# Optimization experiments

Hardware: AMD Instinct MI355X
Metric: run time of the kernel (lower is better)

## Reference

```python
import jax, jax.numpy as jnp
import numpy as np

N, D, C = 8192, 10000, 1000


def setup_inputs() -> dict:
    key = jax.random.key(0)
    k1, k2 = jax.random.split(key)
    # binary {0,1} hypervectors, stored as float32 for efficient GEMM-form Hamming distance
    samples = jax.random.randint(k1, (N, D), 0, 2).astype(jnp.float32)
    classes_hv = jax.random.randint(k2, (C, D), 0, 2).astype(jnp.float32)
    return {"samples": samples, "classes_hv": classes_hv}


def reference(samples, classes_hv):
    # Original: response[i] = sum_d xor(samples[:, d], classes_hv[i, d])  (Hamming distance)
    # For binary a,b: xor(a,b) = a + b - 2*a*b, so the full [N, C] distance matrix is
    # dist = row_sum(samples)[:, None] + row_sum(hv)[None, :] - 2 * samples @ hv.T
    # This replaces the per-class XOR+reduce loop with one GEMM (same math).
    s_sum = jnp.sum(samples, axis=-1)          # [N]
    c_sum = jnp.sum(classes_hv, axis=-1)       # [C]
    cross = jnp.einsum('nd,cd->nc', samples, classes_hv)  # [N, C]
    return s_sum[:, None] + c_sum[None, :] - 2.0 * cross  # [N, C] Hamming distances
```

## Files before the change

### kernel.cpp

```cpp
#include <hip/hip_runtime.h>
#include <stdint.h>

#define N_ROWS 8192
#define C_CLS  1000
#define D_DIM  10000
#define W64P   160
#define W32P   (W64P * 2)
#define DP     (W32P * 32)
#define BKW    16
#define NCHUNK 20

typedef int v4i  __attribute__((ext_vector_type(4)));
typedef int v16i __attribute__((ext_vector_type(16)));

__global__ __launch_bounds__(256) void pack_kernel(
    const float* __restrict__ samples, const float* __restrict__ classes,
    unsigned long long* __restrict__ pA, unsigned long long* __restrict__ pB)
{
    int gwave = (blockIdx.x * 256 + threadIdx.x) >> 6;
    int lane  = threadIdx.x & 63;
    if (gwave >= N_ROWS + C_CLS) return;

    const float* src;
    unsigned long long* dst;
    if (gwave < N_ROWS) {
        src = samples + (size_t)gwave * D_DIM;
        dst = pA + (size_t)gwave * W64P;
    } else {
        int r = gwave - N_ROWS;
        src = classes + (size_t)r * D_DIM;
        dst = pB + (size_t)r * W64P;
    }

    #pragma unroll 4
    for (int w = 0; w < 40; ++w) {
        int idx = w * 256 + lane * 4;
        float4 v = make_float4(0.f, 0.f, 0.f, 0.f);
        if (idx < D_DIM) v = *(const float4*)(src + idx);
        unsigned long long m0 = __ballot(v.x > 0.5f);
        unsigned long long m1 = __ballot(v.y > 0.5f);
        unsigned long long m2 = __ballot(v.z > 0.5f);
        unsigned long long m3 = __ballot(v.w > 0.5f);
        if (lane == 0) {
            uint4 p0, p1;
            p0.x = (uint32_t)m0; p0.y = (uint32_t)(m0 >> 32);
            p0.z = (uint32_t)m1; p0.w = (uint32_t)(m1 >> 32);
            p1.x = (uint32_t)m2; p1.y = (uint32_t)(m2 >> 32);
            p1.z = (uint32_t)m3; p1.w = (uint32_t)(m3 >> 32);
            *(uint4*)(dst + (size_t)w * 4)     = p0;
            *(uint4*)(dst + (size_t)w * 4 + 2) = p1;
        }
    }
}

__global__ __launch_bounds__(256) void hd_kernel(
    const uint32_t* __restrict__ pA, const uint32_t* __restrict__ pB,
    float* __restrict__ out)
{
    __shared__ uint32_t AsT[2][BKW][128];
    __shared__ uint32_t BsT[2][BKW][128];

    const int tid  = threadIdx.x;
    const int row0 = blockIdx.x * 128;
    const int col0 = blockIdx.y * 128;

    const int w    = tid >> 6;
    const int lane = tid & 63;
    const int wy   = w >> 1;
    const int wx   = w & 1;
    const int ln   = lane & 31;
    const int h4   = (lane >> 5) * 4;

    const int srow = tid >> 1;
    const int sq2  = (tid & 1) * 2;
    const uint32_t* gAs = pA + (size_t)(row0 + srow) * W32P + sq2 * 4;
    int gc = col0 + srow; if (gc >= C_CLS) gc = C_CLS - 1;
    const uint32_t* gBs = pB + (size_t)gc * W32P + sq2 * 4;

    uint4 av[2], bv[2];

#define LOADR(ch) do {                                             \
    av[0] = *(const uint4*)(gAs + (ch) * BKW);                     \
    av[1] = *(const uint4*)(gAs + (ch) * BKW + 4);                 \
    bv[0] = *(const uint4*)(gBs + (ch) * BKW);                     \
    bv[1] = *(const uint4*)(gBs + (ch) * BKW + 4);                 \
} while (0)

#define WRITELDS(buf) do {                                         \
    AsT[buf][sq2 * 4 + 0][srow] = av[0].x;                         \
    AsT[buf][sq2 * 4 + 1][srow] = av[0].y;                         \
    AsT[buf][sq2 * 4 + 2][srow] = av[0].z;                         \
    AsT[buf][sq2 * 4 + 3][srow] = av[0].w;                         \
    AsT[buf][sq2 * 4 + 4][srow] = av[1].x;                         \
    AsT[buf][sq2 * 4 + 5][srow] = av[1].y;                         \
    AsT[buf][sq2 * 4 + 6][srow] = av[1].z;                         \
    AsT[buf][sq2 * 4 + 7][srow] = av[1].w;                         \
    BsT[buf][sq2 * 4 + 0][srow] = bv[0].x;                         \
    BsT[buf][sq2 * 4 + 1][srow] = bv[0].y;                         \
    BsT[buf][sq2 * 4 + 2][srow] = bv[0].z;                         \
    BsT[buf][sq2 * 4 + 3][srow] = bv[0].w;                         \
    BsT[buf][sq2 * 4 + 4][srow] = bv[1].x;                         \
    BsT[buf][sq2 * 4 + 5][srow] = bv[1].y;                         \
    BsT[buf][sq2 * 4 + 6][srow] = bv[1].z;                         \
    BsT[buf][sq2 * 4 + 7][srow] = bv[1].w;                         \
} while (0)

#define UNPACK(dst, src) do {                                      \
    uint32_t t_;                                                   \
    t_ = ((src) >> (h4 + 0)) & 0x01010101u;                        \
    dst[0] = (int)((t_ * 0xFEu) ^ 0xFFFFFFFFu);                    \
    t_ = ((src) >> (h4 + 1)) & 0x01010101u;                        \
    dst[1] = (int)((t_ * 0xFEu) ^ 0xFFFFFFFFu);                    \
    t_ = ((src) >> (h4 + 2)) & 0x01010101u;                        \
    dst[2] = (int)((t_ * 0xFEu) ^ 0xFFFFFFFFu);                    \
    t_ = ((src) >> (h4 + 3)) & 0x01010101u;                        \
    dst[3] = (int)((t_ * 0xFEu) ^ 0xFFFFFFFFu);                    \
} while (0)

    v16i acc00 = {}, acc01 = {}, acc10 = {}, acc11 = {};

    LOADR(0);
    WRITELDS(0);
    __syncthreads();

    #pragma unroll 2
    for (int ch = 0; ch < NCHUNK; ++ch) {
        const int cur = ch & 1;
        if (ch + 1 < NCHUNK) LOADR(ch + 1);

        const uint32_t* Ac = &AsT[cur][0][0];
        const uint32_t* Bc = &BsT[cur][0][0];

        #pragma unroll
        for (int s = 0; s < BKW; ++s) {
            uint32_t wa0 = Ac[s * 128 + wy * 64 + ln];
            uint32_t wa1 = Ac[s * 128 + wy * 64 + 32 + ln];
            uint32_t wb0 = Bc[s * 128 + wx * 64 + ln];
            uint32_t wb1 = Bc[s * 128 + wx * 64 + 32 + ln];
            v4i a0, a1, b0, b1;
            UNPACK(a0, wa0);
            UNPACK(a1, wa1);
            UNPACK(b0, wb0);
            UNPACK(b1, wb1);
            acc00 = __builtin_amdgcn_mfma_i32_32x32x32_i8(a0, b0, acc00, 0, 0, 0);
            acc01 = __builtin_amdgcn_mfma_i32_32x32x32_i8(a0, b1, acc01, 0, 0, 0);
            acc10 = __builtin_amdgcn_mfma_i32_32x32x32_i8(a1, b0, acc10, 0, 0, 0);
            acc11 = __builtin_amdgcn_mfma_i32_32x32x32_i8(a1, b1, acc11, 0, 0, 0);
        }

        if (ch + 1 < NCHUNK) {
            WRITELDS((ch + 1) & 1);
            __syncthreads();
        }
    }
#undef LOADR
#undef WRITELDS
#undef UNPACK

    const int mh = h4;
    #pragma unroll
    for (int r = 0; r < 16; ++r) {
        const int m = (r & 3) + 8 * (r >> 2) + mh;
        {
            int grow = row0 + wy * 64 + m;
            int gcol = col0 + wx * 64 + ln;
            if (gcol < C_CLS)
                out[(size_t)grow * C_CLS + gcol] = (float)((DP - acc00[r]) >> 1);
        }
        {
            int grow = row0 + wy * 64 + m;
            int gcol = col0 + wx * 64 + 32 + ln;
            if (gcol < C_CLS)
                out[(size_t)grow * C_CLS + gcol] = (float)((DP - acc01[r]) >> 1);
        }
        {
            int grow = row0 + wy * 64 + 32 + m;
            int gcol = col0 + wx * 64 + ln;
            if (gcol < C_CLS)
                out[(size_t)grow * C_CLS + gcol] = (float)((DP - acc10[r]) >> 1);
        }
        {
            int grow = row0 + wy * 64 + 32 + m;
            int gcol = col0 + wx * 64 + 32 + ln;
            if (gcol < C_CLS)
                out[(size_t)grow * C_CLS + gcol] = (float)((DP - acc11[r]) >> 1);
        }
    }
}

extern "C" void kernel_launch(void* const* d_in, const int* in_sizes, int n_in,
                              void* d_out, int out_size, void* d_ws, size_t ws_size,
                              hipStream_t stream) {
    const float* samples = (const float*)d_in[0];
    const float* classes = (const float*)d_in[1];
    float* out = (float*)d_out;

    unsigned long long* pA = (unsigned long long*)d_ws;
    unsigned long long* pB = pA + (size_t)N_ROWS * W64P;

    int waves  = N_ROWS + C_CLS;
    int blocks = (waves + 3) / 4;
    pack_kernel<<<blocks, 256, 0, stream>>>(samples, classes, pA, pB);

    dim3 grid(N_ROWS / 128, 8);
    hd_kernel<<<grid, 256, 0, stream>>>((const uint32_t*)pA, (const uint32_t*)pB, out);
}
```

Before: 576.7 us.

## Use 0/1 unpack with row popcounts and interleaved LDS layout for Hamming GEMM

The pack kernel now records per-row popcounts, so the GEMM can multiply plain 0/1 bytes instead of ±1 encodings, and the epilogue computes distance as rowsum_a + rowsum_b - 2*dot. This removes the multiply and xor per unpacked word in the inner loop. The LDS tile is re-laid out so each thread stores and reads uint2 pairs of consecutive k-words, halving the number of LDS instructions. In exchange the epilogue does extra global loads of the row sums, and the workspace is assumed to have room for the sum arrays.

```diff
diff --git a/kernel.cpp b/kernel.cpp
--- a/kernel.cpp
+++ b/kernel.cpp
@@ -6,7 +6,6 @@
 #define D_DIM  10000
 #define W64P   160
 #define W32P   (W64P * 2)
-#define DP     (W32P * 32)
 #define BKW    16
 #define NCHUNK 20
 
@@ -15,7 +14,8 @@
 
 __global__ __launch_bounds__(256) void pack_kernel(
     const float* __restrict__ samples, const float* __restrict__ classes,
-    unsigned long long* __restrict__ pA, unsigned long long* __restrict__ pB)
+    unsigned long long* __restrict__ pA, unsigned long long* __restrict__ pB,
+    uint32_t* __restrict__ rsA, uint32_t* __restrict__ rsB)
 {
     int gwave = (blockIdx.x * 256 + threadIdx.x) >> 6;
     int lane  = threadIdx.x & 63;
@@ -23,15 +23,19 @@
 
     const float* src;
     unsigned long long* dst;
+    uint32_t* rsw;
     if (gwave < N_ROWS) {
         src = samples + (size_t)gwave * D_DIM;
         dst = pA + (size_t)gwave * W64P;
+        rsw = rsA + gwave;
     } else {
         int r = gwave - N_ROWS;
         src = classes + (size_t)r * D_DIM;
         dst = pB + (size_t)r * W64P;
-    }
-
+        rsw = rsB + r;
+    }
+
+    uint32_t rs = 0;
     #pragma unroll 4
     for (int w = 0; w < 40; ++w) {
         int idx = w * 256 + lane * 4;
@@ -41,6 +45,7 @@
         unsigned long long m1 = __ballot(v.y > 0.5f);
         unsigned long long m2 = __ballot(v.z > 0.5f);
         unsigned long long m3 = __ballot(v.w > 0.5f);
+        rs += (uint32_t)(__popcll(m0) + __popcll(m1) + __popcll(m2) + __popcll(m3));
         if (lane == 0) {
             uint4 p0, p1;
             p0.x = (uint32_t)m0; p0.y = (uint32_t)(m0 >> 32);
@@ -51,14 +56,16 @@
             *(uint4*)(dst + (size_t)w * 4 + 2) = p1;
         }
     }
+    if (lane == 0) *rsw = rs;
 }
 
 __global__ __launch_bounds__(256) void hd_kernel(
     const uint32_t* __restrict__ pA, const uint32_t* __restrict__ pB,
+    const uint32_t* __restrict__ rsA, const uint32_t* __restrict__ rsB,
     float* __restrict__ out)
 {
-    __shared__ uint32_t AsT[2][BKW][128];
-    __shared__ uint32_t BsT[2][BKW][128];
+    __shared__ uint32_t AsT[2][BKW * 128];
+    __shared__ uint32_t BsT[2][BKW * 128];
 
     const int tid  = threadIdx.x;
     const int row0 = blockIdx.x * 128;
@@ -87,34 +94,23 @@
 } while (0)
 
 #define WRITELDS(buf) do {                                         \
-    AsT[buf][sq2 * 4 + 0][srow] = av[0].x;                         \
-    AsT[buf][sq2 * 4 + 1][srow] = av[0].y;                         \
-    AsT[buf][sq2 * 4 + 2][srow] = av[0].z;                         \
-    AsT[buf][sq2 * 4 + 3][srow] = av[0].w;                         \
-    AsT[buf][sq2 * 4 + 4][srow] = av[1].x;                         \
-    AsT[buf][sq2 * 4 + 5][srow] = av[1].y;                         \
-    AsT[buf][sq2 * 4 + 6][srow] = av[1].z;                         \
-    AsT[buf][sq2 * 4 + 7][srow] = av[1].w;                         \
-    BsT[buf][sq2 * 4 + 0][srow] = bv[0].x;                         \
-    BsT[buf][sq2 * 4 + 1][srow] = bv[0].y;                         \
-    BsT[buf][sq2 * 4 + 2][srow] = bv[0].z;                         \
-    BsT[buf][sq2 * 4 + 3][srow] = bv[0].w;                         \
-    BsT[buf][sq2 * 4 + 4][srow] = bv[1].x;                         \
-    BsT[buf][sq2 * 4 + 5][srow] = bv[1].y;                         \
-    BsT[buf][sq2 * 4 + 6][srow] = bv[1].z;                         \
-    BsT[buf][sq2 * 4 + 7][srow] = bv[1].w;                         \
+    uint32_t* ap_ = &AsT[buf][sq2 * 512 + srow * 2];               \
+    uint32_t* bp_ = &BsT[buf][sq2 * 512 + srow * 2];               \
+    *(uint2*)(ap_      ) = make_uint2(av[0].x, av[0].y);           \
+    *(uint2*)(ap_ + 256) = make_uint2(av[0].z, av[0].w);           \
+    *(uint2*)(ap_ + 512) = make_uint2(av[1].x, av[1].y);           \
+    *(uint2*)(ap_ + 768) = make_uint2(av[1].z, av[1].w);           \
+    *(uint2*)(bp_      ) = make_uint2(bv[0].x, bv[0].y);           \
+    *(uint2*)(bp_ + 256) = make_uint2(bv[0].z, bv[0].w);           \
+    *(uint2*)(bp_ + 512) = make_uint2(bv[1].x, bv[1].y);           \
+    *(uint2*)(bp_ + 768) = make_uint2(bv[1].z, bv[1].w);           \
 } while (0)
 
-#define UNPACK(dst, src) do {                                      \
-    uint32_t t_;                                                   \
-    t_ = ((src) >> (h4 + 0)) & 0x01010101u;                        \
-    dst[0] = (int)((t_ * 0xFEu) ^ 0xFFFFFFFFu);                    \
-    t_ = ((src) >> (h4 + 1)) & 0x01010101u;                        \
-    dst[1] = (int)((t_ * 0xFEu) ^ 0xFFFFFFFFu);                    \
-    t_ = ((src) >> (h4 + 2)) & 0x01010101u;                        \
-    dst[2] = (int)((t_ * 0xFEu) ^ 0xFFFFFFFFu);                    \
-    t_ = ((src) >> (h4 + 3)) & 0x01010101u;                        \
-    dst[3] = (int)((t_ * 0xFEu) ^ 0xFFFFFFFFu);                    \
+#define UNP(dst, src) do {                                         \
+    dst[0] = (int)(((src) >> (h4 + 0)) & 0x01010101u);             \
+    dst[1] = (int)(((src) >> (h4 + 1)) & 0x01010101u);             \
+    dst[2] = (int)(((src) >> (h4 + 2)) & 0x01010101u);             \
+    dst[3] = (int)(((src) >> (h4 + 3)) & 0x01010101u);             \
 } while (0)
 
     v16i acc00 = {}, acc01 = {}, acc10 = {}, acc11 = {};
@@ -128,24 +124,26 @@
         const int cur = ch & 1;
         if (ch + 1 < NCHUNK) LOADR(ch + 1);
 
-        const uint32_t* Ac = &AsT[cur][0][0];
-        const uint32_t* Bc = &BsT[cur][0][0];
+        const uint32_t* Ac = &AsT[cur][0];
+        const uint32_t* Bc = &BsT[cur][0];
 
         #pragma unroll
-        for (int s = 0; s < BKW; ++s) {
-            uint32_t wa0 = Ac[s * 128 + wy * 64 + ln];
-            uint32_t wa1 = Ac[s * 128 + wy * 64 + 32 + ln];
-            uint32_t wb0 = Bc[s * 128 + wx * 64 + ln];
-            uint32_t wb1 = Bc[s * 128 + wx * 64 + 32 + ln];
+        for (int p = 0; p < BKW / 2; ++p) {
+            uint2 wa0 = *(const uint2*)&Ac[p * 256 + (wy * 64 + ln) * 2];
+            uint2 wa1 = *(const uint2*)&Ac[p * 256 + (wy * 64 + 32 + ln) * 2];
+            uint2 wb0 = *(const uint2*)&Bc[p * 256 + (wx * 64 + ln) * 2];
+            uint2 wb1 = *(const uint2*)&Bc[p * 256 + (wx * 64 + 32 + ln) * 2];
             v4i a0, a1, b0, b1;
-            UNPACK(a0, wa0);
-            UNPACK(a1, wa1);
-            UNPACK(b0, wb0);
-            UNPACK(b1, wb1);
+            UNP(a0, wa0.x); UNP(a1, wa1.x); UNP(b0, wb0.x); UNP(b1, wb1.x);
             acc00 = __builtin_amdgcn_mfma_i32_32x32x32_i8(a0, b0, acc00, 0, 0, 0);
             acc01 = __builtin_amdgcn_mfma_i32_32x32x32_i8(a0, b1, acc01, 0, 0, 0);
             acc10 = __builtin_amdgcn_mfma_i32_32x32x32_i8(a1, b0, acc10, 0, 0, 0);
             acc11 = __builtin_amdgcn_mfma_i32_32x32x32_i8(a1, b1, acc11, 0, 0, 0);
+            UNP(a0, wa0.y); UNP(a1, wa1.y); UNP(b0, wb0.y); UNP(b1, wb1.y);
+            acc00 = __builtin_amdgcn_mfma_i32_32x32x32_i8(a0, b0, acc00, 0, 0, 0);
+            acc01 = __builtin_amdgcn_mfma_i32_32x32x32_i8(a0, b1, acc01, 0, 0, 0);
+            acc10 = __builtin_amdgcn_mfma_i32_32x32x32_i8(a1, b0, acc10, 0, 0, 0);
+            acc11 = __builtin_amdgcn_mfma_i32_32x32x32_i8(a1, b1, acc11, 0, 0, 0);
         }
 
         if (ch + 1 < NCHUNK) {
@@ -155,35 +153,30 @@
     }
 #undef LOADR
 #undef WRITELDS
-#undef UNPACK
-
-    const int mh = h4;
+#undef UNP
+
+    const int gcol0 = col0 + wx * 64 + ln;
+    const int gcol1 = gcol0 + 32;
+    const uint32_t rb0 = (gcol0 < C_CLS) ? rsB[gcol0] : 0u;
+    const uint32_t rb1 = (gcol1 < C_CLS) ? rsB[gcol1] : 0u;
     #pragma unroll
     for (int r = 0; r < 16; ++r) {
-        const int m = (r & 3) + 8 * (r >> 2) + mh;
-        {
-            int grow = row0 + wy * 64 + m;
-            int gcol = col0 + wx * 64 + ln;
-            if (gcol < C_CLS)
-                out[(size_t)grow * C_CLS + gcol] = (float)((DP - acc00[r]) >> 1);
-        }
-        {
-            int grow = row0 + wy * 64 + m;
-            int gcol = col0 + wx * 64 + 32 + ln;
-            if (gcol < C_CLS)
-                out[(size_t)grow * C_CLS + gcol] = (float)((DP - acc01[r]) >> 1);
-        }
-        {
-            int grow = row0 + wy * 64 + 32 + m;
-            int gcol = col0 + wx * 64 + ln;
-            if (gcol < C_CLS)
-                out[(size_t)grow * C_CLS + gcol] = (float)((DP - acc10[r]) >> 1);
-        }
-        {
-            int grow = row0 + wy * 64 + 32 + m;
-            int gcol = col0 + wx * 64 + 32 + ln;
-            if (gcol < C_CLS)
-                out[(size_t)grow * C_CLS + gcol] = (float)((DP - acc11[r]) >> 1);
+        const int m     = (r & 3) + 8 * (r >> 2) + h4;
+        const int rowa  = row0 + wy * 64 + m;
+        const int rowb  = rowa + 32;
+        const uint32_t ra0 = rsA[rowa];
+        const uint32_t ra1 = rsA[rowb];
+        if (gcol0 < C_CLS) {
+            out[(size_t)rowa * C_CLS + gcol0] =
+                (float)(int)(ra0 + rb0 - 2u * (uint32_t)acc00[r]);
+            out[(size_t)rowb * C_CLS + gcol0] =
+                (float)(int)(ra1 + rb0 - 2u * (uint32_t)acc10[r]);
+        }
+        if (gcol1 < C_CLS) {
+            out[(size_t)rowa * C_CLS + gcol1] =
+                (float)(int)(ra0 + rb1 - 2u * (uint32_t)acc01[r]);
+            out[(size_t)rowb * C_CLS + gcol1] =
+                (float)(int)(ra1 + rb1 - 2u * (uint32_t)acc11[r]);
         }
     }
 }
@@ -197,11 +190,14 @@
 
     unsigned long long* pA = (unsigned long long*)d_ws;
     unsigned long long* pB = pA + (size_t)N_ROWS * W64P;
+    uint32_t* rsA = (uint32_t*)(pB + (size_t)C_CLS * W64P);
+    uint32_t* rsB = rsA + N_ROWS;
 
     int waves  = N_ROWS + C_CLS;
     int blocks = (waves + 3) / 4;
-    pack_kernel<<<blocks, 256, 0, stream>>>(samples, classes, pA, pB);
+    pack_kernel<<<blocks, 256, 0, stream>>>(samples, classes, pA, pB, rsA, rsB);
 
     dim3 grid(N_ROWS / 128, 8);
-    hd_kernel<<<grid, 256, 0, stream>>>((const uint32_t*)pA, (const uint32_t*)pB, out);
+    hd_kernel<<<grid, 256, 0, stream>>>((const uint32_t*)pA, (const uint32_t*)pB,
+                                        rsA, rsB, out);
 }
```

Result: faster. 543.6 us (-5.7%).
